# Kernel tuning notes

Measured on AMD Instinct MI355X. Metric: run time of the kernel, lower is better.

The kernel has to match this reference:

```python
import jax, jax.numpy as jnp
import numpy as np

N, M, FIN, K, OUT, E = 8, 49152, 64, 6, 64, 393216


def setup_inputs() -> dict:
    key = jax.random.key(0)
    k1, k2, k3, k4, k5, k6 = jax.random.split(key, 6)
    x = jax.random.normal(k1, (N, M, FIN), jnp.float32)
    rows = jax.random.randint(k2, (E,), 0, M, jnp.int32)
    cols = jax.random.randint(k3, (E,), 0, M, jnp.int32)
    vals = jax.random.normal(k4, (E,), jnp.float32) * 0.1  # scaled-Laplacian values
    stdv = 1.0 / np.sqrt(OUT)
    weight = jax.random.uniform(k5, (FIN * K, OUT), jnp.float32, -stdv, stdv)
    bias = jax.random.uniform(k6, (OUT,), jnp.float32, -stdv, stdv)
    return {"x": x, "rows": rows, "cols": cols, "vals": vals,
            "weight": weight, "bias": bias}


def reference(x, rows, cols, vals, weight, bias):
    # x: [N, M, Fin]; L sparse [M, M] in COO (rows, cols, vals)
    n, m, fin = x.shape
    # x0: [M, Fin*N] as in torch permute(1,2,0).view(M, Fin*N)
    x0 = jnp.transpose(x, (1, 2, 0)).reshape(m, fin * n)

    def spmm(X):  # L @ X via gather + segment-sum scatter
        return jax.ops.segment_sum(vals[:, None] * X[cols], rows, num_segments=m)

    xs = [x0]
    if K > 1:
        x1 = spmm(x0)
        xs.append(x1)
        for _ in range(2, K):
            x2 = 2.0 * spmm(x1) - x0
            xs.append(x2)
            x0, x1 = x1, x2

    # stack -> [K, M, Fin, N]; torch then permutes to [N, M, Fin, K] and
    # flattens to (N*M, Fin*K) with Fin outer, K inner: weight row idx = f*K + k
    T = jnp.stack(xs, 0).reshape(K, m, fin, n)
    Wr = weight.reshape(fin, K, OUT)
    out = jnp.einsum('kmfn,fko->nmo', T, Wr) + bias  # [N, M, OUT]
    return jax.nn.elu(out)
```

## Files before the change

kernel.cpp:

```cpp
#include <hip/hip_runtime.h>
#include <hip/hip_bf16.h>
#include <math.h>

#define N_    8
#define M_    49152
#define FIN_  64
#define K_    6
#define OUT_  64
#define E_    393216
#define ROW_  512

typedef __attribute__((ext_vector_type(8))) short bf16x8;
typedef __attribute__((ext_vector_type(4))) float f32x4;

static __device__ __forceinline__ unsigned short f2bf(float f) {
    unsigned u = __float_as_uint(f);
    u += 0x7fff + ((u >> 16) & 1);
    return (unsigned short)(u >> 16);
}
static __device__ __forceinline__ float bfl(unsigned u) { return __uint_as_float(u << 16); }
static __device__ __forceinline__ float bfh(unsigned u) { return __uint_as_float(u & 0xffff0000u); }


__global__ void count_kernel(const int* __restrict__ rows, int* __restrict__ cnt) {
    int e = blockIdx.x * blockDim.x + threadIdx.x;
    if (e < E_) atomicAdd(&cnt[rows[e]], 1);
}

__global__ __launch_bounds__(1024) void scan_kernel(int* __restrict__ cntfill, int* __restrict__ rowptr) {
    __shared__ int wsum[16];
    __shared__ int carry;
    int t = threadIdx.x;
    int lane = t & 63, wid = t >> 6;
    if (t == 0) carry = 0;
    __syncthreads();
    for (int chunk = 0; chunk < M_; chunk += 1024) {
        int v = cntfill[chunk + t];
        int x = v;
        #pragma unroll
        for (int off = 1; off < 64; off <<= 1) {
            int y = __shfl_up(x, off, 64);
            if (lane >= off) x += y;
        }
        if (lane == 63) wsum[wid] = x;
        __syncthreads();
        if (t == 0) {
            int s = carry;
            #pragma unroll
            for (int i = 0; i < 16; ++i) { int c = wsum[i]; wsum[i] = s; s += c; }
            carry = s;
        }
        __syncthreads();
        int excl = wsum[wid] + x - v;
        rowptr[chunk + t]  = excl;
        cntfill[chunk + t] = excl;
        __syncthreads();
    }
    if (t == 0) rowptr[M_] = carry;
}

__global__ void fill_kernel(const int* __restrict__ rows, const int* __restrict__ cols,
                            const float* __restrict__ vals, int* __restrict__ fillpos,
                            int* __restrict__ ecol, float* __restrict__ evalv,
                            int* __restrict__ eidx) {
    int e = blockIdx.x * blockDim.x + threadIdx.x;
    if (e < E_) {
        int r = rows[e];
        int p = atomicAdd(&fillpos[r], 1);
        ecol[p]  = cols[e];
        evalv[p] = vals[e];
        eidx[p]  = e;
    }
}

__global__ void sort_kernel(const int* __restrict__ rowptr, int* __restrict__ ecol,
                            float* __restrict__ evalv, int* __restrict__ eidx) {
    int m = blockIdx.x * blockDim.x + threadIdx.x;
    if (m >= M_) return;
    int s = rowptr[m], e = rowptr[m + 1];
    for (int i = s + 1; i < e; ++i) {
        int ki = eidx[i]; int kc = ecol[i]; float kv = evalv[i];
        int j = i - 1;
        while (j >= s && eidx[j] > ki) {
            eidx[j + 1] = eidx[j]; ecol[j + 1] = ecol[j]; evalv[j + 1] = evalv[j];
            --j;
        }
        eidx[j + 1] = ki; ecol[j + 1] = kc; evalv[j + 1] = kv;
    }
}


__global__ void permute_bf16_kernel(const float* __restrict__ x, unsigned short* __restrict__ T0) {
    int idx = blockIdx.x * blockDim.x + threadIdx.x;
    int f4 = idx & 15, n = (idx >> 4) & 7, m = idx >> 7;
    float4 v = ((const float4*)x)[(size_t)(n * M_ + m) * 16 + f4];
    ushort4 o;
    o.x = f2bf(v.x); o.y = f2bf(v.y); o.z = f2bf(v.z); o.w = f2bf(v.w);
    *(ushort4*)(T0 + (size_t)m * ROW_ + n * 64 + f4 * 4) = o;
}

static __device__ __forceinline__ void fma_u4(float* acc, float v, uint4 u) {
    acc[0] += v * bfl(u.x); acc[1] += v * bfh(u.x);
    acc[2] += v * bfl(u.y); acc[3] += v * bfh(u.y);
    acc[4] += v * bfl(u.z); acc[5] += v * bfh(u.z);
    acc[6] += v * bfl(u.w); acc[7] += v * bfh(u.w);
}

__global__ __launch_bounds__(256) void spmm_bf16_kernel(
        const unsigned short* __restrict__ cur, const unsigned short* __restrict__ prev,
        unsigned short* __restrict__ nxt,
        const int* __restrict__ rowptr, const int* __restrict__ ecol,
        const float* __restrict__ evalv, float alpha, float beta) {
    int t = threadIdx.x;
    int w = t >> 6, l = t & 63;
    int m = blockIdx.x * 4 + w;
    int s = rowptr[m], e = rowptr[m + 1];
    float acc[8] = {0.f, 0.f, 0.f, 0.f, 0.f, 0.f, 0.f, 0.f};
    int i = s;
    for (; i + 1 < e; i += 2) {
        int c0 = ecol[i],     c1 = ecol[i + 1];
        float v0 = evalv[i],  v1 = evalv[i + 1];
        uint4 u0 = *(const uint4*)(cur + (size_t)c0 * ROW_ + l * 8);
        uint4 u1 = *(const uint4*)(cur + (size_t)c1 * ROW_ + l * 8);
        fma_u4(acc, v0, u0);
        fma_u4(acc, v1, u1);
    }
    if (i < e) {
        int c0 = ecol[i];
        float v0 = evalv[i];
        uint4 u0 = *(const uint4*)(cur + (size_t)c0 * ROW_ + l * 8);
        fma_u4(acc, v0, u0);
    }
    #pragma unroll
    for (int j = 0; j < 8; ++j) acc[j] *= alpha;
    if (beta != 0.f) {
        uint4 p = *(const uint4*)(prev + (size_t)m * ROW_ + l * 8);
        acc[0] += beta * bfl(p.x); acc[1] += beta * bfh(p.x);
        acc[2] += beta * bfl(p.y); acc[3] += beta * bfh(p.y);
        acc[4] += beta * bfl(p.z); acc[5] += beta * bfh(p.z);
        acc[6] += beta * bfl(p.w); acc[7] += beta * bfh(p.w);
    }
    uint4 o;
    o.x = (unsigned)f2bf(acc[0]) | ((unsigned)f2bf(acc[1]) << 16);
    o.y = (unsigned)f2bf(acc[2]) | ((unsigned)f2bf(acc[3]) << 16);
    o.z = (unsigned)f2bf(acc[4]) | ((unsigned)f2bf(acc[5]) << 16);
    o.w = (unsigned)f2bf(acc[6]) | ((unsigned)f2bf(acc[7]) << 16);
    *(uint4*)(nxt + (size_t)m * ROW_ + l * 8) = o;
}

__global__ void wprep_kernel(const float* __restrict__ W, unsigned short* __restrict__ Wfrag) {
    int idx = blockIdx.x * blockDim.x + threadIdx.x;
    int i = idx & 7, l = (idx >> 3) & 63, tile = (idx >> 9) & 3, kk = idx >> 11;
    int kcheb = kk >> 1;
    int f = (kk & 1) * 32 + (l >> 4) * 8 + i;
    int o = tile * 16 + (l & 15);
    Wfrag[idx] = f2bf(W[(f * K_ + kcheb) * OUT_ + o]);
}

static __device__ __forceinline__ void epilogue_tile(
        f32x4 acc, int tile, int rbase, int col,
        const float* __restrict__ bias, float* __restrict__ outn) {
    int c = tile * 16 + col;
    float b = bias[c];
    #pragma unroll
    for (int v = 0; v < 4; ++v) {
        float r = acc[v] + b;
        r = r > 0.f ? r : (__expf(r) - 1.f);
        outn[(size_t)(rbase + v) * OUT_ + c] = r;
    }
}

__global__ __launch_bounds__(256) void combine_kernel(
        const unsigned short* __restrict__ Tbase,
        const unsigned short* __restrict__ Wfrag,
        const float* __restrict__ bias, float* __restrict__ out) {
    int n  = blockIdx.y;
    int bm = blockIdx.x;
    int t  = threadIdx.x;
    int w = t >> 6, l = t & 63;
    int m0 = bm * 64 + w * 16;
    int arow = m0 + (l & 15);
    size_t abase = (size_t)arow * ROW_ + n * 64 + (l >> 4) * 8;
    const size_t MROW = (size_t)M_ * ROW_;

    bf16x8 a[12];
    #pragma unroll
    for (int kk = 0; kk < 12; ++kk) {
        const unsigned short* Tk = Tbase + (size_t)(kk >> 1) * MROW;
        a[kk] = *(const bf16x8*)(Tk + abase + (kk & 1) * 32);
    }

    f32x4 acc0 = {0.f, 0.f, 0.f, 0.f};
    f32x4 acc1 = {0.f, 0.f, 0.f, 0.f};
    f32x4 acc2 = {0.f, 0.f, 0.f, 0.f};
    f32x4 acc3 = {0.f, 0.f, 0.f, 0.f};

    #pragma unroll
    for (int kk = 0; kk < 12; ++kk) {
        const unsigned short* wp = Wfrag + ((size_t)(kk * 4) * 64 + l) * 8;
        bf16x8 b0 = *(const bf16x8*)(wp);
        bf16x8 b1 = *(const bf16x8*)(wp + 64 * 8);
        bf16x8 b2 = *(const bf16x8*)(wp + 2 * 64 * 8);
        bf16x8 b3 = *(const bf16x8*)(wp + 3 * 64 * 8);
        acc0 = __builtin_amdgcn_mfma_f32_16x16x32_bf16(a[kk], b0, acc0, 0, 0, 0);
        acc1 = __builtin_amdgcn_mfma_f32_16x16x32_bf16(a[kk], b1, acc1, 0, 0, 0);
        acc2 = __builtin_amdgcn_mfma_f32_16x16x32_bf16(a[kk], b2, acc2, 0, 0, 0);
        acc3 = __builtin_amdgcn_mfma_f32_16x16x32_bf16(a[kk], b3, acc3, 0, 0, 0);
    }

    float* outn = out + (size_t)n * ((size_t)M_ * OUT_);
    int rbase = m0 + (l >> 4) * 4;
    int col = l & 15;
    epilogue_tile(acc0, 0, rbase, col, bias, outn);
    epilogue_tile(acc1, 1, rbase, col, bias, outn);
    epilogue_tile(acc2, 2, rbase, col, bias, outn);
    epilogue_tile(acc3, 3, rbase, col, bias, outn);
}


__global__ void permute_kernel(const float* __restrict__ x, float* __restrict__ A) {
    int idx = blockIdx.x * blockDim.x + threadIdx.x;
    int f4 = idx & 15;
    int n  = (idx >> 4) & 7;
    int m  = idx >> 7;
    float4 v = ((const float4*)x)[(size_t)(n * M_ + m) * 16 + f4];
    ((float4*)A)[idx] = v;
}

__global__ __launch_bounds__(512) void step_kernel(
        const float* __restrict__ cur, float* __restrict__ nxt,
        const float* __restrict__ weight, const float* __restrict__ bias,
        const int* __restrict__ rowptr, const int* __restrict__ ecol,
        const float* __restrict__ evalv, float* __restrict__ out,
        int k, float alpha, float beta, int flags) {
    __shared__ float lds_x[ROW_];
    int m = blockIdx.x;
    int t = threadIdx.x;
    lds_x[t] = cur[(size_t)m * ROW_ + t];
    if (flags & 4) {
        float acc = 0.f;
        int s = rowptr[m], e = rowptr[m + 1];
        for (int i = s; i < e; ++i)
            acc += evalv[i] * cur[(size_t)ecol[i] * ROW_ + t];
        float prevv = (beta != 0.f) ? nxt[(size_t)m * ROW_ + t] : 0.f;
        nxt[(size_t)m * ROW_ + t] = alpha * acc + beta * prevv;
    }
    __syncthreads();
    int n = t >> 6, o = t & 63;
    const float4* lx4 = (const float4*)(lds_x + n * FIN_);
    float acc = 0.f;
    #pragma unroll
    for (int f4 = 0; f4 < 16; ++f4) {
        float4 xq = lx4[f4];
        int fb = f4 * 4;
        acc += xq.x * weight[((fb + 0) * K_ + k) * OUT_ + o];
        acc += xq.y * weight[((fb + 1) * K_ + k) * OUT_ + o];
        acc += xq.z * weight[((fb + 2) * K_ + k) * OUT_ + o];
        acc += xq.w * weight[((fb + 3) * K_ + k) * OUT_ + o];
    }
    size_t oidx = (size_t)n * (M_ * OUT_) + (size_t)m * OUT_ + o;
    float res = (flags & 1) ? acc : (out[oidx] + acc);
    if (flags & 2) {
        res += bias[o];
        res = (res > 0.f) ? res : (expf(res) - 1.f);
    }
    out[oidx] = res;
}


extern "C" void kernel_launch(void* const* d_in, const int* in_sizes, int n_in,
                              void* d_out, int out_size, void* d_ws, size_t ws_size,
                              hipStream_t stream) {
    (void)in_sizes; (void)n_in; (void)out_size;
    const float* x      = (const float*)d_in[0];
    const int*   rows   = (const int*)d_in[1];
    const int*   cols   = (const int*)d_in[2];
    const float* vals   = (const float*)d_in[3];
    const float* weight = (const float*)d_in[4];
    const float* bias   = (const float*)d_in[5];
    float* out = (float*)d_out;

    char* ws = (char*)d_ws;
    size_t off = 0;
    auto alloc = [&](size_t bytes) -> void* {
        void* p = ws + off;
        off += (bytes + 255) & ~(size_t)255;
        return p;
    };

    const size_t tbytes = (size_t)M_ * ROW_ * 2;
    const size_t need_new = 6 * (tbytes + 256) + (M_ + 1) * 4 + M_ * 4
                          + 3 * ((size_t)E_ * 4 + 256) + 24576 * 2 + 4096;

    if (ws_size >= need_new) {
        unsigned short* T[6];
        for (int i = 0; i < 6; ++i) T[i] = (unsigned short*)alloc(tbytes);
        int*   rowptr  = (int*)alloc((size_t)(M_ + 1) * 4);
        int*   fillpos = (int*)alloc((size_t)M_ * 4);
        int*   ecol    = (int*)alloc((size_t)E_ * 4);
        float* evalv   = (float*)alloc((size_t)E_ * 4);
        int*   eidx    = (int*)alloc((size_t)E_ * 4);
        unsigned short* Wfrag = (unsigned short*)alloc(24576 * 2);

        permute_bf16_kernel<<<(M_ * N_ * 16) / 256, 256, 0, stream>>>(x, T[0]);
        hipMemsetAsync(fillpos, 0, (size_t)M_ * 4, stream);
        count_kernel<<<E_ / 256, 256, 0, stream>>>(rows, fillpos);
        scan_kernel<<<1, 1024, 0, stream>>>(fillpos, rowptr);
        fill_kernel<<<E_ / 256, 256, 0, stream>>>(rows, cols, vals, fillpos, ecol, evalv, eidx);
        sort_kernel<<<M_ / 256, 256, 0, stream>>>(rowptr, ecol, evalv, eidx);
        wprep_kernel<<<96, 256, 0, stream>>>(weight, Wfrag);

        spmm_bf16_kernel<<<M_ / 4, 256, 0, stream>>>(T[0], T[0], T[1], rowptr, ecol, evalv, 1.f, 0.f);
        spmm_bf16_kernel<<<M_ / 4, 256, 0, stream>>>(T[1], T[0], T[2], rowptr, ecol, evalv, 2.f, -1.f);
        spmm_bf16_kernel<<<M_ / 4, 256, 0, stream>>>(T[2], T[1], T[3], rowptr, ecol, evalv, 2.f, -1.f);
        spmm_bf16_kernel<<<M_ / 4, 256, 0, stream>>>(T[3], T[2], T[4], rowptr, ecol, evalv, 2.f, -1.f);
        spmm_bf16_kernel<<<M_ / 4, 256, 0, stream>>>(T[4], T[3], T[5], rowptr, ecol, evalv, 2.f, -1.f);

        combine_kernel<<<dim3(M_ / 64, 8), 256, 0, stream>>>(T[0], Wfrag, bias, out);
    } else {
        float* A       = (float*)alloc((size_t)M_ * ROW_ * 4);
        float* B       = (float*)alloc((size_t)M_ * ROW_ * 4);
        int*   rowptr  = (int*)alloc((size_t)(M_ + 1) * 4);
        int*   fillpos = (int*)alloc((size_t)M_ * 4);
        int*   ecol    = (int*)alloc((size_t)E_ * 4);
        float* evalv   = (float*)alloc((size_t)E_ * 4);
        int*   eidx    = (int*)alloc((size_t)E_ * 4);

        permute_kernel<<<(M_ * N_ * 16) / 256, 256, 0, stream>>>(x, A);
        hipMemsetAsync(fillpos, 0, (size_t)M_ * 4, stream);
        count_kernel<<<E_ / 256, 256, 0, stream>>>(rows, fillpos);
        scan_kernel<<<1, 1024, 0, stream>>>(fillpos, rowptr);
        fill_kernel<<<E_ / 256, 256, 0, stream>>>(rows, cols, vals, fillpos, ecol, evalv, eidx);
        sort_kernel<<<M_ / 256, 256, 0, stream>>>(rowptr, ecol, evalv, eidx);

        step_kernel<<<M_, 512, 0, stream>>>(A, B, weight, bias, rowptr, ecol, evalv, out, 0, 1.f, 0.f, 1 | 4);
        step_kernel<<<M_, 512, 0, stream>>>(B, A, weight, bias, rowptr, ecol, evalv, out, 1, 2.f, -1.f, 4);
        step_kernel<<<M_, 512, 0, stream>>>(A, B, weight, bias, rowptr, ecol, evalv, out, 2, 2.f, -1.f, 4);
        step_kernel<<<M_, 512, 0, stream>>>(B, A, weight, bias, rowptr, ecol, evalv, out, 3, 2.f, -1.f, 4);
        step_kernel<<<M_, 512, 0, stream>>>(A, B, weight, bias, rowptr, ecol, evalv, out, 4, 2.f, -1.f, 4);
        step_kernel<<<M_, 512, 0, stream>>>(B, B, weight, bias, rowptr, ecol, evalv, out, 5, 0.f, 0.f, 2);
    }
}
```

Before: 595.0 us.

## Stage weight fragments in LDS for combine and unroll SpMM gather by four

The combine kernel now copies the full bf16 weight fragment buffer (48KB) into shared memory once per block. Each wave then loops over four batch indices for a 16-row tile, reusing the staged weights instead of re-reading them from global memory on every block. The grid shrinks to M/32 one-dimensional blocks. Separately, the SpMM inner loop is unrolled from two to four gathered neighbour rows to keep more loads in flight. The trade-offs are higher LDS use per block, which lowers occupancy, more per-thread work, and more registers in SpMM.

```diff
diff --git a/kernel.cpp b/kernel.cpp
--- a/kernel.cpp
+++ b/kernel.cpp
@@ -117,19 +117,27 @@
     int s = rowptr[m], e = rowptr[m + 1];
     float acc[8] = {0.f, 0.f, 0.f, 0.f, 0.f, 0.f, 0.f, 0.f};
     int i = s;
-    for (; i + 1 < e; i += 2) {
-        int c0 = ecol[i],     c1 = ecol[i + 1];
-        float v0 = evalv[i],  v1 = evalv[i + 1];
+    for (; i + 3 < e; i += 4) {
+        int c0 = ecol[i], c1 = ecol[i+1], c2 = ecol[i+2], c3 = ecol[i+3];
+        float v0 = evalv[i], v1 = evalv[i+1], v2 = evalv[i+2], v3 = evalv[i+3];
         uint4 u0 = *(const uint4*)(cur + (size_t)c0 * ROW_ + l * 8);
         uint4 u1 = *(const uint4*)(cur + (size_t)c1 * ROW_ + l * 8);
-        fma_u4(acc, v0, u0);
-        fma_u4(acc, v1, u1);
+        uint4 u2 = *(const uint4*)(cur + (size_t)c2 * ROW_ + l * 8);
+        uint4 u3 = *(const uint4*)(cur + (size_t)c3 * ROW_ + l * 8);
+        fma_u4(acc, v0, u0); fma_u4(acc, v1, u1);
+        fma_u4(acc, v2, u2); fma_u4(acc, v3, u3);
+    }
+    if (i + 1 < e) {
+        int c0 = ecol[i], c1 = ecol[i+1];
+        float v0 = evalv[i], v1 = evalv[i+1];
+        uint4 u0 = *(const uint4*)(cur + (size_t)c0 * ROW_ + l * 8);
+        uint4 u1 = *(const uint4*)(cur + (size_t)c1 * ROW_ + l * 8);
+        fma_u4(acc, v0, u0); fma_u4(acc, v1, u1);
+        i += 2;
     }
     if (i < e) {
-        int c0 = ecol[i];
-        float v0 = evalv[i];
-        uint4 u0 = *(const uint4*)(cur + (size_t)c0 * ROW_ + l * 8);
-        fma_u4(acc, v0, u0);
+        uint4 u0 = *(const uint4*)(cur + (size_t)ecol[i] * ROW_ + l * 8);
+        fma_u4(acc, evalv[i], u0);
     }
     #pragma unroll
     for (int j = 0; j < 8; ++j) acc[j] *= alpha;
@@ -174,47 +182,58 @@
         const unsigned short* __restrict__ Tbase,
         const unsigned short* __restrict__ Wfrag,
         const float* __restrict__ bias, float* __restrict__ out) {
-    int n  = blockIdx.y;
-    int bm = blockIdx.x;
-    int t  = threadIdx.x;
+    __shared__ unsigned short wlds[24576];
+    int t = threadIdx.x;
+    {
+        const uint4* src = (const uint4*)Wfrag;
+        uint4* dst = (uint4*)wlds;
+        #pragma unroll
+        for (int i = 0; i < 12; ++i)
+            dst[t + 256 * i] = src[t + 256 * i];
+    }
+    __syncthreads();
+
     int w = t >> 6, l = t & 63;
-    int m0 = bm * 64 + w * 16;
+    int rowhalf = w & 1, nhalf = w >> 1;
+    int m0 = blockIdx.x * 32 + rowhalf * 16;
     int arow = m0 + (l & 15);
-    size_t abase = (size_t)arow * ROW_ + n * 64 + (l >> 4) * 8;
     const size_t MROW = (size_t)M_ * ROW_;
-
-    bf16x8 a[12];
-    #pragma unroll
-    for (int kk = 0; kk < 12; ++kk) {
-        const unsigned short* Tk = Tbase + (size_t)(kk >> 1) * MROW;
-        a[kk] = *(const bf16x8*)(Tk + abase + (kk & 1) * 32);
-    }
-
-    f32x4 acc0 = {0.f, 0.f, 0.f, 0.f};
-    f32x4 acc1 = {0.f, 0.f, 0.f, 0.f};
-    f32x4 acc2 = {0.f, 0.f, 0.f, 0.f};
-    f32x4 acc3 = {0.f, 0.f, 0.f, 0.f};
-
-    #pragma unroll
-    for (int kk = 0; kk < 12; ++kk) {
-        const unsigned short* wp = Wfrag + ((size_t)(kk * 4) * 64 + l) * 8;
-        bf16x8 b0 = *(const bf16x8*)(wp);
-        bf16x8 b1 = *(const bf16x8*)(wp + 64 * 8);
-        bf16x8 b2 = *(const bf16x8*)(wp + 2 * 64 * 8);
-        bf16x8 b3 = *(const bf16x8*)(wp + 3 * 64 * 8);
-        acc0 = __builtin_amdgcn_mfma_f32_16x16x32_bf16(a[kk], b0, acc0, 0, 0, 0);
-        acc1 = __builtin_amdgcn_mfma_f32_16x16x32_bf16(a[kk], b1, acc1, 0, 0, 0);
-        acc2 = __builtin_amdgcn_mfma_f32_16x16x32_bf16(a[kk], b2, acc2, 0, 0, 0);
-        acc3 = __builtin_amdgcn_mfma_f32_16x16x32_bf16(a[kk], b3, acc3, 0, 0, 0);
-    }
-
-    float* outn = out + (size_t)n * ((size_t)M_ * OUT_);
+    size_t abase0 = (size_t)arow * ROW_ + (l >> 4) * 8;
     int rbase = m0 + (l >> 4) * 4;
     int col = l & 15;
-    epilogue_tile(acc0, 0, rbase, col, bias, outn);
-    epilogue_tile(acc1, 1, rbase, col, bias, outn);
-    epilogue_tile(acc2, 2, rbase, col, bias, outn);
-    epilogue_tile(acc3, 3, rbase, col, bias, outn);
+
+    #pragma unroll
+    for (int ni = 0; ni < 4; ++ni) {
+        int n = nhalf * 4 + ni;
+        size_t abase = abase0 + n * 64;
+        bf16x8 a[12];
+        #pragma unroll
+        for (int kk = 0; kk < 12; ++kk)
+            a[kk] = *(const bf16x8*)(Tbase + (size_t)(kk >> 1) * MROW + abase + (kk & 1) * 32);
+
+        f32x4 acc0 = {0.f, 0.f, 0.f, 0.f};
+        f32x4 acc1 = {0.f, 0.f, 0.f, 0.f};
+        f32x4 acc2 = {0.f, 0.f, 0.f, 0.f};
+        f32x4 acc3 = {0.f, 0.f, 0.f, 0.f};
+        #pragma unroll
+        for (int kk = 0; kk < 12; ++kk) {
+            const unsigned short* wp = wlds + ((size_t)(kk * 4) * 64 + l) * 8;
+            bf16x8 b0 = *(const bf16x8*)(wp);
+            bf16x8 b1 = *(const bf16x8*)(wp + 512);
+            bf16x8 b2 = *(const bf16x8*)(wp + 1024);
+            bf16x8 b3 = *(const bf16x8*)(wp + 1536);
+            acc0 = __builtin_amdgcn_mfma_f32_16x16x32_bf16(a[kk], b0, acc0, 0, 0, 0);
+            acc1 = __builtin_amdgcn_mfma_f32_16x16x32_bf16(a[kk], b1, acc1, 0, 0, 0);
+            acc2 = __builtin_amdgcn_mfma_f32_16x16x32_bf16(a[kk], b2, acc2, 0, 0, 0);
+            acc3 = __builtin_amdgcn_mfma_f32_16x16x32_bf16(a[kk], b3, acc3, 0, 0, 0);
+        }
+
+        float* outn = out + (size_t)n * ((size_t)M_ * OUT_);
+        epilogue_tile(acc0, 0, rbase, col, bias, outn);
+        epilogue_tile(acc1, 1, rbase, col, bias, outn);
+        epilogue_tile(acc2, 2, rbase, col, bias, outn);
+        epilogue_tile(acc3, 3, rbase, col, bias, outn);
+    }
 }
 
 
@@ -316,7 +335,7 @@
         spmm_bf16_kernel<<<M_ / 4, 256, 0, stream>>>(T[3], T[2], T[4], rowptr, ecol, evalv, 2.f, -1.f);
         spmm_bf16_kernel<<<M_ / 4, 256, 0, stream>>>(T[4], T[3], T[5], rowptr, ecol, evalv, 2.f, -1.f);
 
-        combine_kernel<<<dim3(M_ / 64, 8), 256, 0, stream>>>(T[0], Wfrag, bias, out);
+        combine_kernel<<<M_ / 32, 256, 0, stream>>>(T[0], Wfrag, bias, out);
     } else {
         float* A       = (float*)alloc((size_t)M_ * ROW_ * 4);
         float* B       = (float*)alloc((size_t)M_ * ROW_ * 4);
```

After: 567.5 us. 1.05x faster.
